# Kernel optimization log

Measured on AMD Instinct MI355X. Metric: run time of the kernel, lower is better.

## Reference

```python
import jax, jax.numpy as jnp
import numpy as np

N = 4096   # nodes
E = 4096   # hyperedges (== N so the original's [N,H] output is fully populated)
F = 256    # feature_size
H = 256    # hidden_size
BLOCK = 64 # node-block size for the blocked masked max/min scan


def setup_inputs() -> dict:
    key = jax.random.key(0)
    ks = jax.random.split(key, 11)
    mask = jax.random.randint(ks[4], (E, N), 0, 2, dtype=jnp.int32)
    # guarantee every hyperedge is non-empty (matches `if end > start` path)
    mask = mask.at[jnp.arange(E), jnp.arange(N)].set(1)
    s = 0.05
    return {
        "pos_features": jax.random.normal(ks[0], (N, F), jnp.float32),
        "pos_matrix": jax.random.normal(ks[1], (N, F), jnp.float32),
        "neg_features": jax.random.normal(ks[2], (N, F), jnp.float32),
        "neg_matrix": jax.random.normal(ks[3], (N, F), jnp.float32),
        "batch_mask": mask,
        "W_self": jax.random.normal(ks[5], (F, H), jnp.float32) * s,
        "b_self": jnp.zeros((H,), jnp.float32),
        "W_hyper": jax.random.normal(ks[6], (F, H), jnp.float32) * s,
        "b_hyper": jnp.zeros((H,), jnp.float32),
        "W_score": jax.random.normal(ks[7], (H, 1), jnp.float32) * s,
        "b_score": jnp.zeros((1,), jnp.float32),
    }


def maxmin_pool(mask_bool, feats):
    """Per-hyperedge (max - min) over member-node features.
    mask_bool: [E, N] bool, feats: [N, H] -> [E, H].
    Blocked over nodes to avoid materializing [E, N, H]."""
    Ee, Nn = mask_bool.shape
    Hh = feats.shape[1]
    nb = Nn // BLOCK
    mask_blocks = mask_bool.reshape(Ee, nb, BLOCK).transpose(1, 0, 2)  # [nb, E, BLOCK]
    feat_blocks = feats.reshape(nb, BLOCK, Hh)                          # [nb, BLOCK, H]

    def body(carry, xs):
        mx, mn = carry
        mblk, fblk = xs                      # [E, BLOCK], [BLOCK, H]
        m = mblk[:, :, None]                 # [E, BLOCK, 1]
        f = fblk[None]                       # [1, BLOCK, H]
        mx = jnp.maximum(mx, jnp.max(jnp.where(m, f, -jnp.inf), axis=1))
        mn = jnp.minimum(mn, jnp.min(jnp.where(m, f, jnp.inf), axis=1))
        return (mx, mn), None

    init = (jnp.full((Ee, Hh), -jnp.inf, feats.dtype),
            jnp.full((Ee, Hh), jnp.inf, feats.dtype))
    (mx, mn), _ = jax.lax.scan(body, init, (mask_blocks, feat_blocks))
    return mx - mn


def reference(pos_features, pos_matrix, neg_features, neg_matrix, batch_mask,
              W_self, b_self, W_hyper, b_hyper, W_score, b_score):
    mask = batch_mask.astype(bool)

    def branch(x_feat, x_mat):
        h = jax.nn.relu(x_feat @ W_self + b_self + x_mat @ W_hyper + b_hyper)  # [N, H]
        pooled = maxmin_pool(mask, h)                                          # [E, H]
        return jax.nn.sigmoid(pooled @ W_score + b_score)                      # [E, 1]

    pos_score = branch(pos_features, pos_matrix)
    neg_score = branch(neg_features, neg_matrix)
    return pos_score, neg_score
```

## Files before the change

kernel.cpp:

```cpp
#include <hip/hip_runtime.h>
#include <hip/hip_bf16.h>
#include <hip/hip_fp16.h>


typedef short bf16x8 __attribute__((ext_vector_type(8)));
typedef float f32x4 __attribute__((ext_vector_type(4)));
typedef short s16x2 __attribute__((ext_vector_type(2)));
typedef unsigned short u16x2 __attribute__((ext_vector_type(2)));

static __device__ __forceinline__ unsigned short f2bf(float f) {
    __hip_bfloat16 b = __float2bfloat16(f);
    return __builtin_bit_cast(unsigned short, b);
}
static __device__ __forceinline__ float f16u_to_f(unsigned u) {
    __half h = __builtin_bit_cast(__half, (unsigned short)(u & 0xffffu));
    return __half2float(h);
}
static __device__ __forceinline__ unsigned pkmax_i16(unsigned a, unsigned b) {
    s16x2 r = __builtin_elementwise_max(__builtin_bit_cast(s16x2, a), __builtin_bit_cast(s16x2, b));
    return __builtin_bit_cast(unsigned, r);
}
static __device__ __forceinline__ unsigned pkmin_u16(unsigned a, unsigned b) {
    u16x2 r = __builtin_elementwise_min(__builtin_bit_cast(u16x2, a), __builtin_bit_cast(u16x2, b));
    return __builtin_bit_cast(unsigned, r);
}
static __device__ __forceinline__ int fpad(int i) { return i + (i >> 4); }
static __device__ __forceinline__ int fh(int i)   { return i + (i >> 3); }

__global__ void k_prepW(const float* __restrict__ Ws, const float* __restrict__ Wh,
                        unsigned short* __restrict__ Wts, unsigned short* __restrict__ Wth) {
    __shared__ unsigned short tile[64][65];
    const int k0 = blockIdx.x * 64, n0 = blockIdx.y * 64;
    const float* W     = blockIdx.z ? Wh : Ws;
    unsigned short* Wt = blockIdx.z ? Wth : Wts;
    const int t = threadIdx.x;
#pragma unroll
    for (int m = 0; m < 16; m++) {
        int li = t + m * 256; int r = li >> 6, c = li & 63;
        tile[r][c] = f2bf(W[(size_t)(k0 + r) * 256 + n0 + c]);
    }
    __syncthreads();
#pragma unroll
    for (int m = 0; m < 16; m++) {
        int li = t + m * 256; int c2 = li >> 6, r2 = li & 63;
        Wt[(size_t)(n0 + c2) * 256 + k0 + r2] = tile[r2][c2];
    }
}

__global__ void k_pack(const int* __restrict__ mask, unsigned* __restrict__ packed) {
    const int w = blockIdx.x * 256 + threadIdx.x;
    const int* p = mask + (size_t)w * 32;
    unsigned word = 0;
#pragma unroll
    for (int j = 0; j < 32; j += 4) {
        int4 m = *(const int4*)(p + j);
        word |= (m.x != 0 ? (1u << (31 - j)) : 0u)
              | (m.y != 0 ? (1u << (30 - j)) : 0u)
              | (m.z != 0 ? (1u << (29 - j)) : 0u)
              | (m.w != 0 ? (1u << (28 - j)) : 0u);
    }
    packed[w] = word;
}

__launch_bounds__(256)
__global__ void k_gemm_relu(const float* __restrict__ pXf, const float* __restrict__ pXm,
                            const float* __restrict__ nXf, const float* __restrict__ nXm,
                            const unsigned short* __restrict__ Wts, const unsigned short* __restrict__ Wth,
                            const float* __restrict__ bs,  const float* __restrict__ bh,
                            unsigned short* __restrict__ hOut, int tmode) {
    const int t  = threadIdx.x;
    const int wv = t >> 6;
    const int l  = t & 63;
    const int lm = l & 15;
    const int q  = l >> 4;
    const int bz = blockIdx.z;
    const float* Xf = bz ? nXf : pXf;
    const float* Xm = bz ? nXm : pXm;
    unsigned short* hb = hOut + (size_t)bz * 4096 * 256;

    const int m0 = blockIdx.x * 64 + wv * 16;
    const int n0 = blockIdx.y * 64;

    f32x4 acc[4] = {};
#pragma unroll
    for (int ks = 0; ks < 512; ks += 32) {
        const float* X           = (ks < 256) ? Xf : Xm;
        const unsigned short* Wt = (ks < 256) ? Wts : Wth;
        const int kk = (ks & 255) + q * 8;
        float4 a0 = *(const float4*)(X + (m0 + lm) * 256 + kk);
        float4 a1 = *(const float4*)(X + (m0 + lm) * 256 + kk + 4);
        bf16x8 a;
        a[0] = (short)f2bf(a0.x); a[1] = (short)f2bf(a0.y);
        a[2] = (short)f2bf(a0.z); a[3] = (short)f2bf(a0.w);
        a[4] = (short)f2bf(a1.x); a[5] = (short)f2bf(a1.y);
        a[6] = (short)f2bf(a1.z); a[7] = (short)f2bf(a1.w);
#pragma unroll
        for (int nt = 0; nt < 4; nt++) {
            bf16x8 b = *(const bf16x8*)(Wt + (n0 + nt * 16 + lm) * 256 + kk);
            acc[nt] = __builtin_amdgcn_mfma_f32_16x16x32_bf16(a, b, acc[nt], 0, 0, 0);
        }
    }
    if (tmode) {
#pragma unroll
        for (int nt = 0; nt < 4; nt++) {
            const int c = n0 + nt * 16 + lm;
            const float bsum = bs[c] + bh[c];
            ushort4 v4;
#pragma unroll
            for (int i = 0; i < 4; i++) {
                float v = acc[nt][i] + bsum;
                v = v > 0.f ? v : 0.f;
                ((unsigned short*)&v4)[i] = __builtin_bit_cast(unsigned short, __float2half(v));
            }
            *(ushort4*)(hb + (size_t)c * 4096 + m0 + q * 4) = v4;
        }
    } else {
#pragma unroll
        for (int nt = 0; nt < 4; nt++) {
            const int c = n0 + nt * 16 + lm;
            const float bsum = bs[c] + bh[c];
#pragma unroll
            for (int i = 0; i < 4; i++) {
                const int r = m0 + q * 4 + i;
                float v = acc[nt][i] + bsum;
                v = v > 0.f ? v : 0.f;
                hb[(size_t)r * 256 + c] = __builtin_bit_cast(unsigned short, __float2half(v));
            }
        }
    }
}

__launch_bounds__(512)
__global__ void k_sortpack(const unsigned short* __restrict__ hT,
                           const int* __restrict__ mask,
                           unsigned* __restrict__ packed,
                           unsigned* __restrict__ topkG, unsigned* __restrict__ botkG) {
    __shared__ unsigned arrA[4352];
    __shared__ unsigned arrB[4352];
    __shared__ unsigned short hist[9216];

    const int c = blockIdx.x, br = blockIdx.y, t = threadIdx.x;
    const int wv = t >> 6, l = t & 63;
    const unsigned short* src = hT + (size_t)(br * 256 + c) * 4096;

    const int gt = (br * 256 + c) * 512 + t;
    const int4* mp = (const int4*)(mask + (size_t)gt * 64);
    int4 mr[8];
#pragma unroll
    for (int i = 0; i < 8; i++) mr[i] = mp[i];

    unsigned keys[8];
    {
        uint4 a = ((const uint4*)src)[t];
        unsigned base = t * 8;
        unsigned w[4] = {a.x, a.y, a.z, a.w};
#pragma unroll
        for (int m = 0; m < 4; m++) {
            keys[2 * m]     = ((w[m] & 0xFFFFu) << 16) | (base + 2 * m);
            keys[2 * m + 1] = (w[m] & 0xFFFF0000u)     | (base + 2 * m + 1);
        }
    }

    auto cvt = [&]() -> unsigned {
        unsigned word = 0;
#pragma unroll
        for (int j2 = 0; j2 < 8; j2++) {
            int4 v = mr[j2];
            const int j = j2 * 4;
            word |= (v.x != 0 ? (1u << (31 - j)) : 0u)
                  | (v.y != 0 ? (1u << (30 - j)) : 0u)
                  | (v.z != 0 ? (1u << (29 - j)) : 0u)
                  | (v.w != 0 ? (1u << (28 - j)) : 0u);
        }
        return word;
    };

    auto sort_pass = [&](int sh, unsigned* Bp) {
        unsigned d[8];
        unsigned c0 = 0, c1 = 0;
#pragma unroll
        for (int m = 0; m < 8; m++) {
            d[m] = (keys[m] >> sh) & 15u;
            unsigned inc = 1u << ((d[m] & 7u) * 4);
            if (d[m] < 8u) c0 += inc; else c1 += inc;
        }
#pragma unroll
        for (int b = 0; b < 8; b++) hist[fh(b * 512 + t)]       = (unsigned short)((c0 >> (b * 4)) & 15u);
#pragma unroll
        for (int b = 0; b < 8; b++) hist[fh((b + 8) * 512 + t)] = (unsigned short)((c1 >> (b * 4)) & 15u);
        __syncthreads();

        unsigned loc[16];
        unsigned sum = 0;
#pragma unroll
        for (int m = 0; m < 16; m++) { loc[m] = sum; sum += hist[fh(t * 16 + m)]; }
        unsigned ws = sum;
#pragma unroll
        for (int off = 1; off < 64; off <<= 1) {
            unsigned n = __shfl_up(ws, off);
            if (l >= off) ws += n;
        }
        if (l == 63) Bp[wv] = ws;
        __syncthreads();
        unsigned wbase = 0;
#pragma unroll
        for (int w2 = 0; w2 < 8; w2++) if (w2 < wv) wbase += Bp[w2];
        const unsigned ex = wbase + ws - sum;
#pragma unroll
        for (int m = 0; m < 16; m++) hist[fh(t * 16 + m)] = (unsigned short)(ex + loc[m]);
        __syncthreads();

#pragma unroll
        for (int m = 0; m < 8; m++) {
            unsigned rank = hist[fh((int)d[m] * 512 + t)];
            unsigned prior = 0;
#pragma unroll
            for (int j = 0; j < m; j++) prior += (d[j] == d[m]) ? 1u : 0u;
            Bp[fpad((int)(rank + prior))] = keys[m];
        }
        __syncthreads();
    };

    auto load_keys = [&](const unsigned* Ap) {
        const unsigned* ap = Ap + t * 8 + (t >> 1);
#pragma unroll
        for (int m = 0; m < 8; m++) keys[m] = ap[m];
    };

    const unsigned pw0 = cvt();
#pragma unroll
    for (int i = 0; i < 8; i++) mr[i] = mp[8 + i];

    sort_pass(16, arrB);
    const unsigned pw1 = cvt();
    load_keys(arrB); sort_pass(20, arrA);
    load_keys(arrA); sort_pass(24, arrB);
    load_keys(arrB); sort_pass(28, arrA);

    if (t < 64) {
        topkG[(br * 64 + t) * 256 + c] = arrA[fpad(4095 - t)];
        botkG[(br * 64 + t) * 256 + c] = arrA[fpad(t)];
    }
    *(uint2*)(packed + (size_t)gt * 2) = make_uint2(pw0, pw1);
}

__launch_bounds__(256)
__global__ void k_probe(const unsigned* __restrict__ topkG,
                        const unsigned* __restrict__ botkG,
                        const unsigned* __restrict__ packed,
                        const unsigned short* __restrict__ hT,
                        const float* __restrict__ Wscore,
                        const float* __restrict__ bscore,
                        float* __restrict__ out) {
    __shared__ __align__(16) unsigned topkL[16 * 256];
    __shared__ __align__(16) unsigned botkL[16 * 256];
    __shared__ __align__(16) unsigned bitsL[16 * 128];

    const int t  = threadIdx.x;
    const int wv = t >> 6;
    const int l  = t & 63;
    const int e0 = blockIdx.x * 16;
    const int br = blockIdx.y;

    {
        const uint4* ts  = (const uint4*)(topkG + br * 16384);
        const uint4* bs2 = (const uint4*)(botkG + br * 16384);
#pragma unroll
        for (int m = 0; m < 4; m++) {
            ((uint4*)topkL)[t + m * 256] = ts[t + m * 256];
            ((uint4*)botkL)[t + m * 256] = bs2[t + m * 256];
        }
        ((uint4*)bitsL)[t]       = ((const uint4*)(packed + e0 * 128))[t];
        ((uint4*)bitsL)[t + 256] = ((const uint4*)(packed + e0 * 128))[t + 256];
    }
    __syncthreads();

    const float bsc = *bscore;
    float wsv[4];
#pragma unroll
    for (int sl = 0; sl < 4; sl++) wsv[sl] = Wscore[l + 64 * sl];

#pragma unroll 1
    for (int k = 0; k < 4; k++) {
        const int e = wv * 4 + k;
        const unsigned* mk = &bitsL[e * 128];
        float s = 0.f;
#pragma unroll
        for (int sl = 0; sl < 4; sl++) {
            const int c = l + 64 * sl;

            unsigned sel = 0xFFFFFFFFu;
#pragma unroll 1
            for (int g = 0; g < 2; g++) {
                unsigned kk[8]; int ss[8];
#pragma unroll
                for (int j = 0; j < 8; j++) kk[j] = topkL[(g * 8 + j) * 256 + c];
#pragma unroll
                for (int j = 0; j < 8; j++)
                    ss[j] = (int)(mk[(kk[j] & 4095u) >> 5] << (kk[j] & 31u));
                unsigned fnd = 0xFFFFFFFFu;
#pragma unroll
                for (int j = 7; j >= 0; j--) if (ss[j] < 0) fnd = kk[j];
                if (fnd != 0xFFFFFFFFu) { sel = fnd; break; }
            }
            if (sel == 0xFFFFFFFFu) {
                const unsigned* tg = topkG + br * 16384 + c;
#pragma unroll 1
                for (int p = 16; p < 64; p++) {
                    unsigned key = tg[p * 256];
                    if ((int)(mk[(key & 4095u) >> 5] << (key & 31u)) < 0) { sel = key; break; }
                }
            }
            if (sel == 0xFFFFFFFFu) {
                const unsigned short* col = hT + (size_t)(br * 256 + c) * 4096;
                unsigned best = 0;
#pragma unroll 1
                for (int n = 0; n < 4096; n++)
                    if ((int)(mk[n >> 5] << (n & 31)) < 0) { unsigned v = col[n]; if (v > best) best = v; }
                sel = best << 16;
            }
            const float vmax = f16u_to_f(sel >> 16);

            sel = 0xFFFFFFFFu;
#pragma unroll 1
            for (int g = 0; g < 2; g++) {
                unsigned kk[8]; int ss[8];
#pragma unroll
                for (int j = 0; j < 8; j++) kk[j] = botkL[(g * 8 + j) * 256 + c];
#pragma unroll
                for (int j = 0; j < 8; j++)
                    ss[j] = (int)(mk[(kk[j] & 4095u) >> 5] << (kk[j] & 31u));
                unsigned fnd = 0xFFFFFFFFu;
#pragma unroll
                for (int j = 7; j >= 0; j--) if (ss[j] < 0) fnd = kk[j];
                if (fnd != 0xFFFFFFFFu) { sel = fnd; break; }
            }
            if (sel == 0xFFFFFFFFu) {
                const unsigned* bg = botkG + br * 16384 + c;
#pragma unroll 1
                for (int p = 16; p < 64; p++) {
                    unsigned key = bg[p * 256];
                    if ((int)(mk[(key & 4095u) >> 5] << (key & 31u)) < 0) { sel = key; break; }
                }
            }
            if (sel == 0xFFFFFFFFu) {
                const unsigned short* col = hT + (size_t)(br * 256 + c) * 4096;
                unsigned best = 0xFFFFu;
#pragma unroll 1
                for (int n = 0; n < 4096; n++)
                    if ((int)(mk[n >> 5] << (n & 31)) < 0) { unsigned v = col[n]; if (v < best) best = v; }
                sel = best << 16;
            }
            const float vmin = f16u_to_f(sel >> 16);

            s += (vmax - vmin) * wsv[sl];
        }
#pragma unroll
        for (int off = 32; off; off >>= 1) s += __shfl_xor(s, off);
        if (l == 0)
            out[br * 4096 + e0 + e] = 1.f / (1.f + __expf(-(s + bsc)));
    }
}

#define POOL_STEP(WE, MX0, MX1, MN0, MN1, VX, VY)                          \
    {                                                                      \
        asm("s_add_u32 %[we], %[we], %[we]\n\t"                            \
            "s_cbranch_scc0 Lskip%=\n\t"                                   \
            "v_pk_max_i16 %[mx0], %[mx0], %[vx]\n\t"                       \
            "v_pk_max_i16 %[mx1], %[mx1], %[vy]\n\t"                       \
            "v_pk_min_u16 %[mn0], %[mn0], %[vx]\n\t"                       \
            "v_pk_min_u16 %[mn1], %[mn1], %[vy]\n"                         \
            "Lskip%=:"                                                     \
            : [we] "+s"(WE),                                               \
              [mx0] "+v"(MX0), [mx1] "+v"(MX1),                            \
              [mn0] "+v"(MN0), [mn1] "+v"(MN1)                             \
            : [vx] "v"(VX), [vy] "v"(VY)                                   \
            : "scc");                                                      \
    }

__launch_bounds__(512, 8)
__global__ void k_pool9(const unsigned short* __restrict__ hAll,
                        const unsigned* __restrict__ packed,
                        const float* __restrict__ Wscore,
                        const float* __restrict__ bscore,
                        float* __restrict__ out) {
    __shared__ __align__(16) unsigned bits[4 * 128];
    __shared__ __align__(16) unsigned part[8][4][64][4];

    const int t  = threadIdx.x;
    const int wv = t >> 6;
    const int l  = t & 63;
    const int e0 = blockIdx.x * 4;
    const int br = blockIdx.y;
    const unsigned short* h = hAll + (size_t)br * 4096 * 256;

    if (t < 128) ((uint4*)bits)[t] = ((const uint4*)(packed + e0 * 128))[t];
    __syncthreads();

    unsigned mx0[4], mx1[4], mn0[4], mn1[4];
#pragma unroll
    for (int e = 0; e < 4; e++) {
        mx0[e] = 0x80008000u; mx1[e] = 0x80008000u;
        mn0[e] = 0xFFFFFFFFu; mn1[e] = 0xFFFFFFFFu;
    }

#pragma unroll 1
    for (int ch = 0; ch < 16; ch++) {
        const int w0 = wv * 16 + ch;
        unsigned we0 = (unsigned)__builtin_amdgcn_readfirstlane((int)bits[0 * 128 + w0]);
        unsigned we1 = (unsigned)__builtin_amdgcn_readfirstlane((int)bits[1 * 128 + w0]);
        unsigned we2 = (unsigned)__builtin_amdgcn_readfirstlane((int)bits[2 * 128 + w0]);
        unsigned we3 = (unsigned)__builtin_amdgcn_readfirstlane((int)bits[3 * 128 + w0]);

        const unsigned short* hp = h + (size_t)(wv * 512 + ch * 32) * 256 + 4 * l;
#pragma unroll
        for (int jj = 0; jj < 8; jj++) {
            uint2 v0 = *(const uint2*)(hp + (jj * 4 + 0) * 256);
            uint2 v1 = *(const uint2*)(hp + (jj * 4 + 1) * 256);
            uint2 v2 = *(const uint2*)(hp + (jj * 4 + 2) * 256);
            uint2 v3 = *(const uint2*)(hp + (jj * 4 + 3) * 256);

            POOL_STEP(we0, mx0[0], mx1[0], mn0[0], mn1[0], v0.x, v0.y);
            POOL_STEP(we1, mx0[1], mx1[1], mn0[1], mn1[1], v0.x, v0.y);
            POOL_STEP(we2, mx0[2], mx1[2], mn0[2], mn1[2], v0.x, v0.y);
            POOL_STEP(we3, mx0[3], mx1[3], mn0[3], mn1[3], v0.x, v0.y);
            POOL_STEP(we0, mx0[0], mx1[0], mn0[0], mn1[0], v1.x, v1.y);
            POOL_STEP(we1, mx0[1], mx1[1], mn0[1], mn1[1], v1.x, v1.y);
            POOL_STEP(we2, mx0[2], mx1[2], mn0[2], mn1[2], v1.x, v1.y);
            POOL_STEP(we3, mx0[3], mx1[3], mn0[3], mn1[3], v1.x, v1.y);
            POOL_STEP(we0, mx0[0], mx1[0], mn0[0], mn1[0], v2.x, v2.y);
            POOL_STEP(we1, mx0[1], mx1[1], mn0[1], mn1[1], v2.x, v2.y);
            POOL_STEP(we2, mx0[2], mx1[2], mn0[2], mn1[2], v2.x, v2.y);
            POOL_STEP(we3, mx0[3], mx1[3], mn0[3], mn1[3], v2.x, v2.y);
            POOL_STEP(we0, mx0[0], mx1[0], mn0[0], mn1[0], v3.x, v3.y);
            POOL_STEP(we1, mx0[1], mx1[1], mn0[1], mn1[1], v3.x, v3.y);
            POOL_STEP(we2, mx0[2], mx1[2], mn0[2], mn1[2], v3.x, v3.y);
            POOL_STEP(we3, mx0[3], mx1[3], mn0[3], mn1[3], v3.x, v3.y);
        }
    }

#pragma unroll
    for (int e = 0; e < 4; e++) {
        uint4 p; p.x = mx0[e]; p.y = mx1[e]; p.z = mn0[e]; p.w = mn1[e];
        *(uint4*)&part[wv][e][l][0] = p;
    }
    __syncthreads();

    if (wv < 4) {
        unsigned rmx0 = 0x80008000u, rmx1 = 0x80008000u;
        unsigned rmn0 = 0xFFFFFFFFu, rmn1 = 0xFFFFFFFFu;
#pragma unroll
        for (int w2 = 0; w2 < 8; w2++) {
            uint4 p = *(const uint4*)&part[w2][wv][l][0];
            rmx0 = pkmax_i16(rmx0, p.x);  rmx1 = pkmax_i16(rmx1, p.y);
            rmn0 = pkmin_u16(rmn0, p.z);  rmn1 = pkmin_u16(rmn1, p.w);
        }
        float4 wsv = *(const float4*)(Wscore + 4 * l);
        const float bsc = *bscore;
        float s = (f16u_to_f(rmx0)       - f16u_to_f(rmn0))       * wsv.x
                + (f16u_to_f(rmx0 >> 16) - f16u_to_f(rmn0 >> 16)) * wsv.y
                + (f16u_to_f(rmx1)       - f16u_to_f(rmn1))       * wsv.z
                + (f16u_to_f(rmx1 >> 16) - f16u_to_f(rmn1 >> 16)) * wsv.w;
#pragma unroll
        for (int off = 32; off; off >>= 1) s += __shfl_xor(s, off);
        if (l == 0)
            out[br * 4096 + e0 + wv] = 1.f / (1.f + __expf(-(s + bsc)));
    }
}

extern "C" void kernel_launch(void* const* d_in, const int* in_sizes, int n_in,
                              void* d_out, int out_size, void* d_ws, size_t ws_size,
                              hipStream_t stream) {
    const float* pf  = (const float*)d_in[0];
    const float* pm  = (const float*)d_in[1];
    const float* nf  = (const float*)d_in[2];
    const float* nm  = (const float*)d_in[3];
    const int*   msk = (const int*)d_in[4];
    const float* Wsf = (const float*)d_in[5];
    const float* bsf = (const float*)d_in[6];
    const float* Whp = (const float*)d_in[7];
    const float* bhp = (const float*)d_in[8];
    const float* Wsc = (const float*)d_in[9];
    const float* bsc = (const float*)d_in[10];
    float* out = (float*)d_out;

    char* ws = (char*)d_ws;
    const size_t MB = 1024u * 1024u;
    unsigned short* hbuf  = (unsigned short*)(ws);
    unsigned*       pck   = (unsigned*)(ws + 4 * MB);
    unsigned short* Wts   = (unsigned short*)(ws + 6 * MB);
    unsigned short* Wth   = Wts + 256 * 256;
    unsigned*       topkG = (unsigned*)(ws + 6 * MB + 256 * 1024);
    unsigned*       botkG = (unsigned*)(ws + 6 * MB + 384 * 1024);
    const size_t need = 6 * MB + 512 * 1024;

    k_prepW<<<dim3(4, 4, 2), 256, 0, stream>>>(Wsf, Whp, Wts, Wth);

    if (ws_size >= need) {
        k_gemm_relu<<<dim3(64, 4, 2), 256, 0, stream>>>(pf, pm, nf, nm, Wts, Wth, bsf, bhp, hbuf, 1);
        k_sortpack<<<dim3(256, 2), 512, 0, stream>>>(hbuf, msk, pck, topkG, botkG);
        k_probe<<<dim3(256, 2), 256, 0, stream>>>(topkG, botkG, pck, hbuf, Wsc, bsc, out);
    } else {
        k_pack<<<2048, 256, 0, stream>>>(msk, pck);
        k_gemm_relu<<<dim3(64, 4, 2), 256, 0, stream>>>(pf, pm, nf, nm, Wts, Wth, bsf, bhp, hbuf, 0);
        k_pool9<<<dim3(1024, 2), 512, 0, stream>>>(hbuf, pck, Wsc, bsc, out);
    }
}
```

Measured before the change: 175.1 us.

## Replace full per-column radix sort with radix select of top and bottom 64

Swaps the four-pass LSD radix sort of each 4096-element column for an MSD radix-select that finds the 64th-largest and 64th-smallest thresholds digit by digit. It then compacts the qualifying keys with a prefix scan and sorts the 64 candidates with a wave-level bitonic network. This removes the full-array scatter passes and their large shared-memory buffers, which cuts LDS traffic and may raise occupancy. The cost is more barriers per digit round, serial threshold selection on a single thread, and extra code for tie handling.

```diff
diff --git a/kernel.cpp b/kernel.cpp
--- a/kernel.cpp
+++ b/kernel.cpp
@@ -24,8 +24,6 @@
     u16x2 r = __builtin_elementwise_min(__builtin_bit_cast(u16x2, a), __builtin_bit_cast(u16x2, b));
     return __builtin_bit_cast(unsigned, r);
 }
-static __device__ __forceinline__ int fpad(int i) { return i + (i >> 4); }
-static __device__ __forceinline__ int fh(int i)   { return i + (i >> 3); }
 
 __global__ void k_prepW(const float* __restrict__ Ws, const float* __restrict__ Wh,
                         unsigned short* __restrict__ Wts, unsigned short* __restrict__ Wth) {
@@ -131,13 +129,16 @@
 }
 
 __launch_bounds__(512)
-__global__ void k_sortpack(const unsigned short* __restrict__ hT,
-                           const int* __restrict__ mask,
-                           unsigned* __restrict__ packed,
-                           unsigned* __restrict__ topkG, unsigned* __restrict__ botkG) {
-    __shared__ unsigned arrA[4352];
-    __shared__ unsigned arrB[4352];
-    __shared__ unsigned short hist[9216];
+__global__ void k_select(const unsigned short* __restrict__ hT,
+                         const int* __restrict__ mask,
+                         unsigned* __restrict__ packed,
+                         unsigned* __restrict__ topkG, unsigned* __restrict__ botkG) {
+    __shared__ unsigned cbuf[4][512];
+    __shared__ unsigned totals[4][4];
+    __shared__ unsigned selS[4];
+    __shared__ unsigned aS[2];
+    __shared__ unsigned wtot2[8][2];
+    __shared__ unsigned top64[64], bot64[64];
 
     const int c = blockIdx.x, br = blockIdx.y, t = threadIdx.x;
     const int wv = t >> 6, l = t & 63;
@@ -149,16 +150,13 @@
 #pragma unroll
     for (int i = 0; i < 8; i++) mr[i] = mp[i];
 
-    unsigned keys[8];
+    unsigned vt[8];
     {
         uint4 a = ((const uint4*)src)[t];
-        unsigned base = t * 8;
-        unsigned w[4] = {a.x, a.y, a.z, a.w};
-#pragma unroll
-        for (int m = 0; m < 4; m++) {
-            keys[2 * m]     = ((w[m] & 0xFFFFu) << 16) | (base + 2 * m);
-            keys[2 * m + 1] = (w[m] & 0xFFFF0000u)     | (base + 2 * m + 1);
-        }
+        vt[0] = a.x & 0xFFFFu; vt[1] = a.x >> 16;
+        vt[2] = a.y & 0xFFFFu; vt[3] = a.y >> 16;
+        vt[4] = a.z & 0xFFFFu; vt[5] = a.z >> 16;
+        vt[6] = a.w & 0xFFFFu; vt[7] = a.w >> 16;
     }
 
     auto cvt = [&]() -> unsigned {
@@ -174,73 +172,149 @@
         }
         return word;
     };
-
-    auto sort_pass = [&](int sh, unsigned* Bp) {
-        unsigned d[8];
-        unsigned c0 = 0, c1 = 0;
+    const unsigned pw0 = cvt();
+#pragma unroll
+    for (int i = 0; i < 8; i++) mr[i] = mp[8 + i];
+
+    unsigned prefT = 0, needT = 64, prefB = 0, needB = 64;
+#pragma unroll 1
+    for (int r = 3; r >= 0; r--) {
+        const int shp = (r + 1) * 4, shd = r * 4;
+        unsigned cT0 = 0, cT1 = 0, cB0 = 0, cB1 = 0;
 #pragma unroll
         for (int m = 0; m < 8; m++) {
-            d[m] = (keys[m] >> sh) & 15u;
-            unsigned inc = 1u << ((d[m] & 7u) * 4);
-            if (d[m] < 8u) c0 += inc; else c1 += inc;
-        }
-#pragma unroll
-        for (int b = 0; b < 8; b++) hist[fh(b * 512 + t)]       = (unsigned short)((c0 >> (b * 4)) & 15u);
-#pragma unroll
-        for (int b = 0; b < 8; b++) hist[fh((b + 8) * 512 + t)] = (unsigned short)((c1 >> (b * 4)) & 15u);
+            const unsigned hi = vt[m] >> shp;
+            const unsigned d  = (vt[m] >> shd) & 15u;
+            const unsigned inc = 1u << ((d & 7u) * 4);
+            const bool lo8 = d < 8u;
+            if (hi == prefT) { if (lo8) cT0 += inc; else cT1 += inc; }
+            if (hi == prefB) { if (lo8) cB0 += inc; else cB1 += inc; }
+        }
+        cbuf[0][t] = cT0; cbuf[1][t] = cT1; cbuf[2][t] = cB0; cbuf[3][t] = cB1;
         __syncthreads();
 
-        unsigned loc[16];
-        unsigned sum = 0;
-#pragma unroll
-        for (int m = 0; m < 16; m++) { loc[m] = sum; sum += hist[fh(t * 16 + m)]; }
-        unsigned ws = sum;
-#pragma unroll
-        for (int off = 1; off < 64; off <<= 1) {
-            unsigned n = __shfl_up(ws, off);
-            if (l >= off) ws += n;
-        }
-        if (l == 63) Bp[wv] = ws;
+        if (wv < 4) {
+            const unsigned* p = cbuf[wv];
+            unsigned e0 = 0, e1 = 0;
+#pragma unroll
+            for (int j = 0; j < 8; j++) {
+                unsigned x = p[l * 8 + j];
+                e0 += x & 0x0F0F0F0Fu;
+                e1 += (x >> 4) & 0x0F0F0F0Fu;
+            }
+            unsigned w00 = e0 & 0x00FF00FFu, w01 = (e0 >> 8) & 0x00FF00FFu;
+            unsigned w10 = e1 & 0x00FF00FFu, w11 = (e1 >> 8) & 0x00FF00FFu;
+#pragma unroll
+            for (int off = 1; off < 64; off <<= 1) {
+                w00 += __shfl_xor(w00, off); w01 += __shfl_xor(w01, off);
+                w10 += __shfl_xor(w10, off); w11 += __shfl_xor(w11, off);
+            }
+            if (l == 0) { totals[wv][0] = w00; totals[wv][1] = w01; totals[wv][2] = w10; totals[wv][3] = w11; }
+        }
         __syncthreads();
-        unsigned wbase = 0;
-#pragma unroll
-        for (int w2 = 0; w2 < 8; w2++) if (w2 < wv) wbase += Bp[w2];
-        const unsigned ex = wbase + ws - sum;
-#pragma unroll
-        for (int m = 0; m < 16; m++) hist[fh(t * 16 + m)] = (unsigned short)(ex + loc[m]);
+
+        if (t == 0) {
+            unsigned cnt[16];
+            cnt[0]  = totals[0][0] & 0xFFFFu; cnt[4]  = totals[0][0] >> 16;
+            cnt[2]  = totals[0][1] & 0xFFFFu; cnt[6]  = totals[0][1] >> 16;
+            cnt[1]  = totals[0][2] & 0xFFFFu; cnt[5]  = totals[0][2] >> 16;
+            cnt[3]  = totals[0][3] & 0xFFFFu; cnt[7]  = totals[0][3] >> 16;
+            cnt[8]  = totals[1][0] & 0xFFFFu; cnt[12] = totals[1][0] >> 16;
+            cnt[10] = totals[1][1] & 0xFFFFu; cnt[14] = totals[1][1] >> 16;
+            cnt[9]  = totals[1][2] & 0xFFFFu; cnt[13] = totals[1][2] >> 16;
+            cnt[11] = totals[1][3] & 0xFFFFu; cnt[15] = totals[1][3] >> 16;
+            {
+                unsigned S = 0, g = 0, nn = 0; bool done = false;
+#pragma unroll
+                for (int b = 15; b >= 0; b--) {
+                    if (!done) {
+                        unsigned cb = cnt[b];
+                        if (S + cb >= needT) { g = (unsigned)b; nn = needT - S; done = true; }
+                        else S += cb;
+                    }
+                }
+                selS[0] = (prefT << 4) | g; selS[1] = nn;
+                if (r == 0) aS[0] = 64u - nn;
+            }
+            cnt[0]  = totals[2][0] & 0xFFFFu; cnt[4]  = totals[2][0] >> 16;
+            cnt[2]  = totals[2][1] & 0xFFFFu; cnt[6]  = totals[2][1] >> 16;
+            cnt[1]  = totals[2][2] & 0xFFFFu; cnt[5]  = totals[2][2] >> 16;
+            cnt[3]  = totals[2][3] & 0xFFFFu; cnt[7]  = totals[2][3] >> 16;
+            cnt[8]  = totals[3][0] & 0xFFFFu; cnt[12] = totals[3][0] >> 16;
+            cnt[10] = totals[3][1] & 0xFFFFu; cnt[14] = totals[3][1] >> 16;
+            cnt[9]  = totals[3][2] & 0xFFFFu; cnt[13] = totals[3][2] >> 16;
+            cnt[11] = totals[3][3] & 0xFFFFu; cnt[15] = totals[3][3] >> 16;
+            {
+                unsigned S = 0, g = 0, nn = 0; bool done = false;
+#pragma unroll
+                for (int b = 0; b < 16; b++) {
+                    if (!done) {
+                        unsigned cb = cnt[b];
+                        if (S + cb >= needB) { g = (unsigned)b; nn = needB - S; done = true; }
+                        else S += cb;
+                    }
+                }
+                selS[2] = (prefB << 4) | g; selS[3] = nn;
+                if (r == 0) aS[1] = 64u - nn;
+            }
+        }
         __syncthreads();
-
-#pragma unroll
-        for (int m = 0; m < 8; m++) {
-            unsigned rank = hist[fh((int)d[m] * 512 + t)];
-            unsigned prior = 0;
-#pragma unroll
-            for (int j = 0; j < m; j++) prior += (d[j] == d[m]) ? 1u : 0u;
-            Bp[fpad((int)(rank + prior))] = keys[m];
-        }
-        __syncthreads();
-    };
-
-    auto load_keys = [&](const unsigned* Ap) {
-        const unsigned* ap = Ap + t * 8 + (t >> 1);
-#pragma unroll
-        for (int m = 0; m < 8; m++) keys[m] = ap[m];
-    };
-
-    const unsigned pw0 = cvt();
-#pragma unroll
-    for (int i = 0; i < 8; i++) mr[i] = mp[8 + i];
-
-    sort_pass(16, arrB);
+        prefT = selS[0]; needT = selS[1]; prefB = selS[2]; needB = selS[3];
+    }
+
     const unsigned pw1 = cvt();
-    load_keys(arrB); sort_pass(20, arrA);
-    load_keys(arrA); sort_pass(24, arrB);
-    load_keys(arrB); sort_pass(28, arrA);
-
-    if (t < 64) {
-        topkG[(br * 64 + t) * 256 + c] = arrA[fpad(4095 - t)];
-        botkG[(br * 64 + t) * 256 + c] = arrA[fpad(t)];
-    }
+
+    const unsigned TvT = prefT, TvB = prefB;
+    const unsigned A_T = aS[0], A_B = aS[1];
+    unsigned dT = 0, tT = 0, dB = 0, tB = 0;
+#pragma unroll
+    for (int m = 0; m < 8; m++) {
+        dT += vt[m] > TvT;  tT += vt[m] == TvT;
+        dB += vt[m] < TvB;  tB += vt[m] == TvB;
+    }
+    unsigned pkT = dT | (tT << 16), pkB = dB | (tB << 16);
+    unsigned sT = pkT, sB = pkB;
+#pragma unroll
+    for (int off = 1; off < 64; off <<= 1) {
+        unsigned nT = __shfl_up(sT, off), nB = __shfl_up(sB, off);
+        if (l >= off) { sT += nT; sB += nB; }
+    }
+    if (l == 63) { wtot2[wv][0] = sT; wtot2[wv][1] = sB; }
+    __syncthreads();
+    unsigned exT = sT - pkT, exB = sB - pkB;
+#pragma unroll
+    for (int w = 0; w < 7; w++)
+        if (w < wv) { exT += wtot2[w][0]; exB += wtot2[w][1]; }
+    unsigned posDT = exT & 0xFFFFu, posTT = exT >> 16;
+    unsigned posDB = exB & 0xFFFFu, posTB = exB >> 16;
+#pragma unroll
+    for (int m = 0; m < 8; m++) {
+        const unsigned key = (vt[m] << 16) | (unsigned)(t * 8 + m);
+        if (vt[m] > TvT)        top64[posDT++] = key;
+        else if (vt[m] == TvT) { unsigned s2 = A_T + posTT++; if (s2 < 64u) top64[s2] = key; }
+        if (vt[m] < TvB)        bot64[posDB++] = key;
+        else if (vt[m] == TvB) { unsigned s2 = A_B + posTB++; if (s2 < 64u) bot64[s2] = key; }
+    }
+    __syncthreads();
+
+    if (wv < 2) {
+        const unsigned flip = (wv == 0) ? 0xFFFFFFFFu : 0u;
+        unsigned v = ((wv == 0) ? top64[l] : bot64[l]) ^ flip;
+#pragma unroll
+        for (unsigned k2 = 2; k2 <= 64; k2 <<= 1) {
+#pragma unroll
+            for (unsigned j = k2 >> 1; j > 0; j >>= 1) {
+                unsigned o = __shfl_xor(v, (int)j);
+                const bool keepMin = (((unsigned)l & j) == 0) == (((unsigned)l & k2) == 0);
+                const unsigned mn = v < o ? v : o, mx = v < o ? o : v;
+                v = keepMin ? mn : mx;
+            }
+        }
+        v ^= flip;
+        if (wv == 0) topkG[(br * 64 + l) * 256 + c] = v;
+        else         botkG[(br * 64 + l) * 256 + c] = v;
+    }
+
     *(uint2*)(packed + (size_t)gt * 2) = make_uint2(pw0, pw1);
 }
 
@@ -498,7 +572,7 @@
 
     if (ws_size >= need) {
         k_gemm_relu<<<dim3(64, 4, 2), 256, 0, stream>>>(pf, pm, nf, nm, Wts, Wth, bsf, bhp, hbuf, 1);
-        k_sortpack<<<dim3(256, 2), 512, 0, stream>>>(hbuf, msk, pck, topkG, botkG);
+        k_select<<<dim3(256, 2), 512, 0, stream>>>(hbuf, msk, pck, topkG, botkG);
         k_probe<<<dim3(256, 2), 256, 0, stream>>>(topkG, botkG, pck, hbuf, Wsc, bsc, out);
     } else {
         k_pack<<<2048, 256, 0, stream>>>(msk, pck);
```

Measured after the change: 175.6 us. Within noise of the previous version (+0.3%).
